# Kernel tuning notes

Hardware: AMD Instinct MI355X
Metric: run time of the kernel (lower is better)

The kernel has to match this reference:

```python
import jax, jax.numpy as jnp
import numpy as np

N, NQ = 65536, 256


def _interleave(x, q):
    # x: [n, nq, 6], q: [n, nq, 3] -> [n, nq, 9]
    return jnp.concatenate([
        x[:, :, 0:2], q[:, :, 0:1],
        x[:, :, 2:4], q[:, :, 1:2],
        x[:, :, 4:6], q[:, :, 2:3],
    ], axis=2)


def _conv_k3s3(v, W, b):
    # Conv1d(kernel=3, stride=3): [n, c, 9] -> [n, o, 3]
    n, c, L = v.shape
    g = L // 3
    vr = v.reshape(n, c, g, 3)  # [n, c, groups, k]
    return jnp.einsum('ncgk,ock->nog', vr, W) + b[None, :, None]


def setup_inputs() -> dict:
    key = jax.random.key(0)
    ks = jax.random.split(key, 5)
    s = 1.0 / np.sqrt(NQ * 3)
    return {
        'x': jax.random.normal(ks[0], (N, NQ, 6), jnp.float32),
        'q': jax.random.normal(ks[1], (N, NQ, 3), jnp.float32),
        'W1': jax.random.uniform(ks[2], (NQ, NQ, 3), jnp.float32, -s, s),
        'b1': jnp.zeros((NQ,), jnp.float32),
        'W2': jax.random.uniform(ks[3], (NQ, NQ, 3), jnp.float32, -s, s),
        'b2': jnp.zeros((NQ,), jnp.float32),
        'W3': jax.random.uniform(ks[4], (NQ, NQ, 3), jnp.float32, -s, s),
        'b3': jnp.zeros((NQ,), jnp.float32),
    }


def reference(x, q, W1, b1, W2, b2, W3, b3):
    q1 = q
    q = jax.nn.relu(_conv_k3s3(_interleave(x, q), W1, b1))
    q = jax.nn.relu(_conv_k3s3(_interleave(x, q), W2, b2))
    q = _conv_k3s3(_interleave(x, q), W3, b3)
    return jax.nn.relu(q + q1)
```

## Files before the change

kernel.cpp:

```cpp
#include <hip/hip_runtime.h>


#define NR   65536
#define CH   256
#define MB   64
#define KT   32
#define NKT  24
#define AROW 768

typedef _Float16 f16;
typedef _Float16 f16x2 __attribute__((ext_vector_type(2)));
typedef _Float16 f16x8 __attribute__((ext_vector_type(8)));
typedef float    f32x4 __attribute__((ext_vector_type(4)));

__global__ __launch_bounds__(256)
void prep_w(const float* __restrict__ W1, const float* __restrict__ W2,
            const float* __restrict__ W3, f16* __restrict__ ws)
{
    const int bid = blockIdx.x;
    const int l = bid / NKT, kt = bid % NKT;
    const float* W = (l == 0) ? W1 : (l == 1) ? W2 : W3;
    const int o = threadIdx.x;
    f16* img = ws + (size_t)bid * (CH * KT);
    #pragma unroll
    for (int ks = 0; ks < KT; ++ks) {
        const int kg = kt * KT + ks;
        int c, kk;
        if (kg < 512) { c = kg >> 1;  kk = kg & 1; }
        else          { c = kg - 512; kk = 2; }
        const float w = W[((size_t)o * CH + c) * 3 + kk];
        img[((ks >> 3) << 11) + (o << 3) + (ks & 7)] = (f16)w;
    }
}

__device__ __forceinline__ void gld_lds16(const void* g, void* l) {
    __builtin_amdgcn_global_load_lds(
        (const __attribute__((address_space(1))) unsigned int*)g,
        (__attribute__((address_space(3))) unsigned int*)l, 16, 0, 0);
}

__global__ __launch_bounds__(256, 1)
void qjrb_mfma(const float* __restrict__ x, const float* __restrict__ q,
               const f16* __restrict__ wsW,
               const float* __restrict__ b1, const float* __restrict__ b2,
               const float* __restrict__ b3, float* __restrict__ out)
{
    __shared__ __align__(16) f16 A[MB * AROW];
    __shared__ __align__(16) f16 Wb[2][CH * KT];

    const int tid = threadIdx.x;
    const int n0  = blockIdx.x * MB;
    const int lan = tid & 63;
    const int wv  = tid >> 6;
    const int lr  = lan & 15;
    const int lq  = lan >> 4;

    for (int g = 0; g < 3; ++g) {
        {
            const char* src = (const char*)wsW;
            char* dst = (char*)&Wb[0][0];
            #pragma unroll
            for (int i = 0; i < 4; ++i)
                gld_lds16(src + tid * 16 + i * 4096, dst + tid * 16 + i * 4096);
        }
        {
            const int c = tid;
            const float* xp = x + ((size_t)n0 * CH + c) * 6 + 2 * g;
            const float* qp = q + ((size_t)n0 * CH + c) * 3 + g;
            #pragma unroll 4
            for (int r = 0; r < MB; ++r) {
                const float2 xx = *(const float2*)(xp + (size_t)r * CH * 6);
                const float  qq = qp[(size_t)r * CH * 3];
                const int sw = r & 7;
                f16x2 hx = { (f16)xx.x, (f16)xx.y };
                *(f16x2*)&A[r * AROW + (((c >> 2) ^ sw) << 3) + ((c & 3) << 1)] = hx;
                A[r * AROW + ((64 + ((c >> 3) ^ sw)) << 3) + (c & 7)] = (f16)qq;
            }
        }

        for (int l = 0; l < 3; ++l) {
            const float* bl = (l == 0) ? b1 : (l == 1) ? b2 : b3;
            f32x4 acc[4][4];
            #pragma unroll
            for (int nt = 0; nt < 4; ++nt) {
                const float bv = bl[wv * 64 + nt * 16 + lr];
                #pragma unroll
                for (int mt = 0; mt < 4; ++mt)
                    acc[mt][nt] = (f32x4){bv, bv, bv, bv};
            }
            __syncthreads();

            int cur = 0;
            for (int kt = 0; kt < NKT; ++kt) {
                if (kt < NKT - 1 || l < 2) {
                    const int nl  = (kt < NKT - 1) ? l : l + 1;
                    const int nkt = (kt < NKT - 1) ? kt + 1 : 0;
                    const char* src = (const char*)wsW + ((size_t)nl * NKT + nkt) * 16384;
                    char* dst = (char*)&Wb[cur ^ 1][0];
                    #pragma unroll
                    for (int i = 0; i < 4; ++i)
                        gld_lds16(src + tid * 16 + i * 4096, dst + tid * 16 + i * 4096);
                }
                f16x8 a[4], b[4];
                #pragma unroll
                for (int mt = 0; mt < 4; ++mt) {
                    const int m = mt * 16 + lr;
                    a[mt] = *(const f16x8*)&A[m * AROW + ((((kt << 2) + lq) ^ (lr & 7)) << 3)];
                }
                #pragma unroll
                for (int nt = 0; nt < 4; ++nt) {
                    const int o = wv * 64 + nt * 16 + lr;
                    b[nt] = *(const f16x8*)&Wb[cur][(lq << 11) + (o << 3)];
                }
                #pragma unroll
                for (int mt = 0; mt < 4; ++mt)
                    #pragma unroll
                    for (int nt = 0; nt < 4; ++nt)
                        acc[mt][nt] = __builtin_amdgcn_mfma_f32_16x16x32_f16(
                            a[mt], b[nt], acc[mt][nt], 0, 0, 0);
                __syncthreads();
                cur ^= 1;
            }

            if (l < 2) {
                #pragma unroll
                for (int mt = 0; mt < 4; ++mt) {
                    #pragma unroll
                    for (int i = 0; i < 4; ++i) {
                        const int m = mt * 16 + lq * 4 + i;
                        const int sw = m & 7;
                        #pragma unroll
                        for (int nt = 0; nt < 4; ++nt) {
                            const int o = wv * 64 + nt * 16 + lr;
                            A[m * AROW + ((64 + ((o >> 3) ^ sw)) << 3) + (o & 7)] =
                                (f16)fmaxf(acc[mt][nt][i], 0.f);
                        }
                    }
                }
            } else {
                #pragma unroll
                for (int mt = 0; mt < 4; ++mt) {
                    #pragma unroll
                    for (int i = 0; i < 4; ++i) {
                        const int m = mt * 16 + lq * 4 + i;
                        #pragma unroll
                        for (int nt = 0; nt < 4; ++nt) {
                            const int o = wv * 64 + nt * 16 + lr;
                            const size_t idx = (((size_t)(n0 + m)) * CH + o) * 3 + g;
                            out[idx] = fmaxf(acc[mt][nt][i] + q[idx], 0.f);
                        }
                    }
                }
            }
        }
        __syncthreads();
    }
}

extern "C" void kernel_launch(void* const* d_in, const int* in_sizes, int n_in,
                              void* d_out, int out_size, void* d_ws, size_t ws_size,
                              hipStream_t stream)
{
    const float* x  = (const float*)d_in[0];
    const float* q  = (const float*)d_in[1];
    const float* W1 = (const float*)d_in[2];
    const float* b1 = (const float*)d_in[3];
    const float* W2 = (const float*)d_in[4];
    const float* b2 = (const float*)d_in[5];
    const float* W3 = (const float*)d_in[6];
    const float* b3 = (const float*)d_in[7];

    if (ws_size < (size_t)3 * NKT * 16384) return;
    f16* ws = (f16*)d_ws;

    hipLaunchKernelGGL(prep_w, dim3(3 * NKT), dim3(256), 0, stream, W1, W2, W3, ws);
    hipLaunchKernelGGL(qjrb_mfma, dim3(NR / MB), dim3(256), 0, stream,
                       x, q, ws, b1, b2, b3, (float*)d_out);
}
```

Before: 1.922 ms.

## Stream weights directly into registers and use 8 waves with accumulated final outputs

Drops the LDS double-buffered weight staging (global_load_lds plus a barrier per k-step). Each wave now loads its weight fragments straight from global/L2 into registers, prefetching one k-step ahead. The block grows to 512 threads in a 2x4 wave grid, each wave computing 32 rows by 64 outputs, with launch bounds allowing 2 blocks per CU. Final-layer accumulators for all three groups are held in registers so the output write happens once, covering all three g values together. This removes most barriers and gives more waves for latency hiding, but repeats weight loads from L2 per wave, lowers per-wave reuse, and raises register pressure.

```diff
diff --git a/kernel.cpp b/kernel.cpp
--- a/kernel.cpp
+++ b/kernel.cpp
@@ -4,9 +4,7 @@
 #define NR   65536
 #define CH   256
 #define MB   64
-#define KT   32
 #define NKT  24
-#define AROW 768
 
 typedef _Float16 f16;
 typedef _Float16 f16x2 __attribute__((ext_vector_type(2)));
@@ -21,10 +19,10 @@
     const int l = bid / NKT, kt = bid % NKT;
     const float* W = (l == 0) ? W1 : (l == 1) ? W2 : W3;
     const int o = threadIdx.x;
-    f16* img = ws + (size_t)bid * (CH * KT);
+    f16* img = ws + (size_t)bid * 8192;
     #pragma unroll
-    for (int ks = 0; ks < KT; ++ks) {
-        const int kg = kt * KT + ks;
+    for (int ks = 0; ks < 32; ++ks) {
+        const int kg = kt * 32 + ks;
         int c, kk;
         if (kg < 512) { c = kg >> 1;  kk = kg & 1; }
         else          { c = kg - 512; kk = 2; }
@@ -33,128 +31,137 @@
     }
 }
 
-__device__ __forceinline__ void gld_lds16(const void* g, void* l) {
-    __builtin_amdgcn_global_load_lds(
-        (const __attribute__((address_space(1))) unsigned int*)g,
-        (__attribute__((address_space(3))) unsigned int*)l, 16, 0, 0);
-}
+#define KLOOP(WL, ACC0, ACC1)                                                  \
+  {                                                                            \
+    f16x8 wcur[4], wnxt[4];                                                    \
+    _Pragma("unroll")                                                          \
+    for (int nt = 0; nt < 4; ++nt)                                             \
+        wcur[nt] = *(const f16x8*)((WL) + wboff + nt * 128);                   \
+    _Pragma("unroll")                                                          \
+    for (int kt = 0; kt < NKT; ++kt) {                                         \
+        if (kt < NKT - 1) {                                                    \
+            _Pragma("unroll")                                                  \
+            for (int nt = 0; nt < 4; ++nt)                                     \
+                wnxt[nt] = *(const f16x8*)((WL) + (kt + 1) * 8192 + wboff + nt * 128); \
+        }                                                                      \
+        const int ak = abase + ((((kt << 2) + lq) << 3) ^ aswz);               \
+        const f16x8 a0v = *(const f16x8*)&A[ak];                               \
+        const f16x8 a1v = *(const f16x8*)&A[ak + 16 * 768];                    \
+        _Pragma("unroll")                                                      \
+        for (int nt = 0; nt < 4; ++nt) {                                       \
+            ACC0[nt] = __builtin_amdgcn_mfma_f32_16x16x32_f16(a0v, wcur[nt], ACC0[nt], 0, 0, 0); \
+            ACC1[nt] = __builtin_amdgcn_mfma_f32_16x16x32_f16(a1v, wcur[nt], ACC1[nt], 0, 0, 0); \
+        }                                                                      \
+        _Pragma("unroll")                                                      \
+        for (int nt = 0; nt < 4; ++nt) wcur[nt] = wnxt[nt];                    \
+    }                                                                          \
+  }
 
-__global__ __launch_bounds__(256, 1)
+__global__ __launch_bounds__(512, 2)
 void qjrb_mfma(const float* __restrict__ x, const float* __restrict__ q,
                const f16* __restrict__ wsW,
                const float* __restrict__ b1, const float* __restrict__ b2,
                const float* __restrict__ b3, float* __restrict__ out)
 {
-    __shared__ __align__(16) f16 A[MB * AROW];
-    __shared__ __align__(16) f16 Wb[2][CH * KT];
+    __shared__ __align__(16) f16 A[MB * 768];
 
     const int tid = threadIdx.x;
-    const int n0  = blockIdx.x * MB;
     const int lan = tid & 63;
     const int wv  = tid >> 6;
+    const int wr  = (wv >> 2) << 5;
+    const int wc  = (wv & 3) << 6;
     const int lr  = lan & 15;
     const int lq  = lan >> 4;
+    const int n0  = blockIdx.x * MB;
 
+    float bf0[4], bf1[4], bf2[4];
+    #pragma unroll
+    for (int nt = 0; nt < 4; ++nt) {
+        bf0[nt] = b1[wc + nt * 16 + lr];
+        bf1[nt] = b2[wc + nt * 16 + lr];
+        bf2[nt] = b3[wc + nt * 16 + lr];
+    }
+
+    const int wboff = lq * 2048 + (wc + lr) * 8;
+    const int abase = (wr + lr) * 768;
+    const int aswz  = (lr & 7) << 3;
+
+    f32x4 accO[3][2][4];
+
+    #pragma unroll
     for (int g = 0; g < 3; ++g) {
+        __syncthreads();
         {
-            const char* src = (const char*)wsW;
-            char* dst = (char*)&Wb[0][0];
-            #pragma unroll
-            for (int i = 0; i < 4; ++i)
-                gld_lds16(src + tid * 16 + i * 4096, dst + tid * 16 + i * 4096);
-        }
-        {
-            const int c = tid;
-            const float* xp = x + ((size_t)n0 * CH + c) * 6 + 2 * g;
-            const float* qp = q + ((size_t)n0 * CH + c) * 3 + g;
-            #pragma unroll 4
-            for (int r = 0; r < MB; ++r) {
-                const float2 xx = *(const float2*)(xp + (size_t)r * CH * 6);
-                const float  qq = qp[(size_t)r * CH * 3];
-                const int sw = r & 7;
+            const int c  = tid & 255;
+            const int rb = (tid >> 8) << 5;
+            const float* xp = x + ((size_t)(n0 + rb) * CH + c) * 6 + 2 * g;
+            const float* qp = q + ((size_t)(n0 + rb) * CH + c) * 3 + g;
+            #pragma unroll 8
+            for (int r = 0; r < 32; ++r) {
+                const float2 xx = *(const float2*)(xp + (size_t)r * (CH * 6));
+                const float  qq = qp[(size_t)r * (CH * 3)];
+                const int row = rb + r, sw = row & 7;
                 f16x2 hx = { (f16)xx.x, (f16)xx.y };
-                *(f16x2*)&A[r * AROW + (((c >> 2) ^ sw) << 3) + ((c & 3) << 1)] = hx;
-                A[r * AROW + ((64 + ((c >> 3) ^ sw)) << 3) + (c & 7)] = (f16)qq;
-            }
-        }
-
-        for (int l = 0; l < 3; ++l) {
-            const float* bl = (l == 0) ? b1 : (l == 1) ? b2 : b3;
-            f32x4 acc[4][4];
-            #pragma unroll
-            for (int nt = 0; nt < 4; ++nt) {
-                const float bv = bl[wv * 64 + nt * 16 + lr];
-                #pragma unroll
-                for (int mt = 0; mt < 4; ++mt)
-                    acc[mt][nt] = (f32x4){bv, bv, bv, bv};
-            }
-            __syncthreads();
-
-            int cur = 0;
-            for (int kt = 0; kt < NKT; ++kt) {
-                if (kt < NKT - 1 || l < 2) {
-                    const int nl  = (kt < NKT - 1) ? l : l + 1;
-                    const int nkt = (kt < NKT - 1) ? kt + 1 : 0;
-                    const char* src = (const char*)wsW + ((size_t)nl * NKT + nkt) * 16384;
-                    char* dst = (char*)&Wb[cur ^ 1][0];
-                    #pragma unroll
-                    for (int i = 0; i < 4; ++i)
-                        gld_lds16(src + tid * 16 + i * 4096, dst + tid * 16 + i * 4096);
-                }
-                f16x8 a[4], b[4];
-                #pragma unroll
-                for (int mt = 0; mt < 4; ++mt) {
-                    const int m = mt * 16 + lr;
-                    a[mt] = *(const f16x8*)&A[m * AROW + ((((kt << 2) + lq) ^ (lr & 7)) << 3)];
-                }
-                #pragma unroll
-                for (int nt = 0; nt < 4; ++nt) {
-                    const int o = wv * 64 + nt * 16 + lr;
-                    b[nt] = *(const f16x8*)&Wb[cur][(lq << 11) + (o << 3)];
-                }
-                #pragma unroll
-                for (int mt = 0; mt < 4; ++mt)
-                    #pragma unroll
-                    for (int nt = 0; nt < 4; ++nt)
-                        acc[mt][nt] = __builtin_amdgcn_mfma_f32_16x16x32_f16(
-                            a[mt], b[nt], acc[mt][nt], 0, 0, 0);
-                __syncthreads();
-                cur ^= 1;
-            }
-
-            if (l < 2) {
-                #pragma unroll
-                for (int mt = 0; mt < 4; ++mt) {
-                    #pragma unroll
-                    for (int i = 0; i < 4; ++i) {
-                        const int m = mt * 16 + lq * 4 + i;
-                        const int sw = m & 7;
-                        #pragma unroll
-                        for (int nt = 0; nt < 4; ++nt) {
-                            const int o = wv * 64 + nt * 16 + lr;
-                            A[m * AROW + ((64 + ((o >> 3) ^ sw)) << 3) + (o & 7)] =
-                                (f16)fmaxf(acc[mt][nt][i], 0.f);
-                        }
-                    }
-                }
-            } else {
-                #pragma unroll
-                for (int mt = 0; mt < 4; ++mt) {
-                    #pragma unroll
-                    for (int i = 0; i < 4; ++i) {
-                        const int m = mt * 16 + lq * 4 + i;
-                        #pragma unroll
-                        for (int nt = 0; nt < 4; ++nt) {
-                            const int o = wv * 64 + nt * 16 + lr;
-                            const size_t idx = (((size_t)(n0 + m)) * CH + o) * 3 + g;
-                            out[idx] = fmaxf(acc[mt][nt][i] + q[idx], 0.f);
-                        }
-                    }
-                }
+                *(f16x2*)&A[row * 768 + (((c >> 2) ^ sw) << 3) + ((c & 3) << 1)] = hx;
+                A[row * 768 + ((64 + ((c >> 3) ^ sw)) << 3) + (c & 7)] = (f16)qq;
             }
         }
         __syncthreads();
+
+        #pragma unroll
+        for (int l = 0; l < 2; ++l) {
+            const f16* Wl = wsW + (size_t)l * NKT * 8192;
+            f32x4 acc[2][4];
+            #pragma unroll
+            for (int nt = 0; nt < 4; ++nt) {
+                const float bv = (l == 0) ? bf0[nt] : bf1[nt];
+                acc[0][nt] = (f32x4){bv, bv, bv, bv};
+                acc[1][nt] = (f32x4){bv, bv, bv, bv};
+            }
+            KLOOP(Wl, acc[0], acc[1]);
+            __syncthreads();
+            #pragma unroll
+            for (int mt = 0; mt < 2; ++mt)
+                #pragma unroll
+                for (int i = 0; i < 4; ++i) {
+                    const int m = wr + mt * 16 + lq * 4 + i;
+                    const int sw = m & 7;
+                    #pragma unroll
+                    for (int nt = 0; nt < 4; ++nt) {
+                        const int o = wc + nt * 16 + lr;
+                        A[m * 768 + ((64 + ((o >> 3) ^ sw)) << 3) + (o & 7)] =
+                            (f16)fmaxf(acc[mt][nt][i], 0.f);
+                    }
+                }
+            __syncthreads();
+        }
+
+        {
+            const f16* Wl = wsW + (size_t)2 * NKT * 8192;
+            #pragma unroll
+            for (int nt = 0; nt < 4; ++nt) {
+                const float bv = bf2[nt];
+                accO[g][0][nt] = (f32x4){bv, bv, bv, bv};
+                accO[g][1][nt] = (f32x4){bv, bv, bv, bv};
+            }
+            KLOOP(Wl, accO[g][0], accO[g][1]);
+        }
     }
+
+    #pragma unroll
+    for (int mt = 0; mt < 2; ++mt)
+        #pragma unroll
+        for (int i = 0; i < 4; ++i) {
+            const int n = n0 + wr + mt * 16 + lq * 4 + i;
+            #pragma unroll
+            for (int nt = 0; nt < 4; ++nt) {
+                const int o = wc + nt * 16 + lr;
+                const size_t base = ((size_t)n * CH + o) * 3;
+                #pragma unroll
+                for (int g3 = 0; g3 < 3; ++g3)
+                    out[base + g3] = fmaxf(accO[g3][mt][nt][i] + q[base + g3], 0.f);
+            }
+        }
 }
 
 extern "C" void kernel_launch(void* const* d_in, const int* in_sizes, int n_in,
@@ -174,6 +181,6 @@
     f16* ws = (f16*)d_ws;
 
     hipLaunchKernelGGL(prep_w, dim3(3 * NKT), dim3(256), 0, stream, W1, W2, W3, ws);
-    hipLaunchKernelGGL(qjrb_mfma, dim3(NR / MB), dim3(256), 0, stream,
+    hipLaunchKernelGGL(qjrb_mfma, dim3(NR / MB), dim3(512), 0, stream,
                        x, q, ws, b1, b2, b3, (float*)d_out);
 }
```

Measured after the change: 1.875 ms. -2.4%, faster.
